# Kernel optimization log

Measured on AMD Instinct MI355X. Metric: run time of the kernel, lower is better.

## Reference

```python
import jax, jax.numpy as jnp
import numpy as np

N, E, C, H, L = 20000, 200000, 64, 4, 2
L0_IN, E_IN, L0_OUT = 65, 15, 64
HC = H * C
EPS = 1e-5  # InstanceNorm1d default eps
NEG_SLOPE = 0.01  # F.leaky_relu default used by DGL EGATConv


def setup_inputs() -> dict:
    key = jax.random.key(0)
    ks = jax.random.split(key, 16)
    def s(k, shape, fan):
        return (jax.random.normal(k, shape, jnp.float32) / np.float32(np.sqrt(fan)))
    return {
        "x": jax.random.normal(ks[0], (N, L0_IN), jnp.float32),
        "efeat": jax.random.normal(ks[1], (E, E_IN), jnp.float32),
        "src": jax.random.randint(ks[2], (E,), 0, N, dtype=jnp.int32),
        "dst": jax.random.randint(ks[3], (E,), 0, N, dtype=jnp.int32),
        "Wn0": s(ks[4], (L0_IN, C), L0_IN),
        "bn0": jnp.zeros((C,), jnp.float32),
        "We0": s(ks[5], (E_IN, C), E_IN),
        "be0": jnp.zeros((C,), jnp.float32),
        "Wnode": s(ks[6], (L, C, HC), C),
        "bnode": jnp.zeros((L, HC), jnp.float32),
        "Wni": s(ks[7], (L, C, HC), C),
        "Wnj": s(ks[8], (L, C, HC), C),
        "Wfij": s(ks[9], (L, C, HC), C),
        "attn": s(ks[10], (L, H, C), C),
        "bias_e": jnp.zeros((L, HC), jnp.float32),
        "Wf": s(ks[11], (C, L0_OUT), C),
        "bf": jnp.zeros((L0_OUT,), jnp.float32),
    }


def _inorm(x):
    # InstanceNorm1d on a 2D [rows, channels] tensor == per-row normalization
    m = jnp.mean(x, axis=-1, keepdims=True)
    v = jnp.var(x, axis=-1, keepdims=True)
    return (x - m) * jax.lax.rsqrt(v + EPS)


def reference(x, efeat, src, dst, Wn0, bn0, We0, be0, Wnode, bnode,
              Wni, Wnj, Wfij, attn, bias_e, Wf, bf):
    h = x @ Wn0 + bn0        # [N, C]
    f = efeat @ We0 + be0    # [E, C]
    for l in range(L):
        # edge feature update: f_out = fc_ni(h)[src] + fc_nj(h)[dst] + fc_fij(f) + bias
        f_out = (h @ Wni[l])[src] + (h @ Wnj[l])[dst] + f @ Wfij[l] + bias_e[l]  # [E, HC]
        e = jax.nn.leaky_relu(f_out, NEG_SLOPE).reshape(E, H, C)
        score = jnp.einsum('ehc,hc->eh', e, attn[l])  # [E, H]
        # edge softmax over incoming edges of each destination node
        smax = jax.ops.segment_max(score, dst, num_segments=N)
        w = jnp.exp(score - smax[dst])
        denom = jax.ops.segment_sum(w, dst, num_segments=N)
        a = w / denom[dst]                                # [E, H]
        hproj = (h @ Wnode[l] + bnode[l]).reshape(N, H, C)
        msg = hproj[src] * a[:, :, None]                  # [E, H, C]
        h_new = jax.ops.segment_sum(msg, dst, num_segments=N)  # [N, H, C]
        # mean over heads -> InstanceNorm -> ELU
        h = jax.nn.elu(_inorm(jnp.mean(h_new, axis=1)))
        f = jax.nn.elu(_inorm(jnp.mean(f_out.reshape(E, H, C), axis=1)))
    return h @ Wf + bf
```

## Files before the change

### kernel.cpp

```cpp
#include <hip/hip_runtime.h>
#include <cmath>

#define NN 20000
#define NE 200000
#define SCAN_BLOCKS 79
#define EBLK 3125
#define EBLK_P 391

typedef __attribute__((ext_vector_type(8))) short bf16x8;
typedef __attribute__((ext_vector_type(4))) float f32x4;
typedef unsigned int uint;

__device__ __forceinline__ float4 ld4(const float* p){ return *(const float4*)p; }

__device__ __forceinline__ uint packbf(float a, float b) {
  uint ua = __float_as_uint(a);
  uint ub = __float_as_uint(b);
  ua = (ua + 0x7fffu + ((ua >> 16) & 1u)) >> 16;
  ub = (ub + 0x7fffu + ((ub >> 16) & 1u)) >> 16;
  return ua | (ub << 16);
}
__device__ __forceinline__ float4 up4(uint2 u) {
  return make_float4(__uint_as_float(u.x << 16), __uint_as_float(u.x & 0xffff0000u),
                     __uint_as_float(u.y << 16), __uint_as_float(u.y & 0xffff0000u));
}

__global__ void gemm16_bf16(const float* __restrict__ A, const float* __restrict__ B,
                            const float* __restrict__ bias, uint2* __restrict__ O,
                            int M, int K, const int* __restrict__ map) {
  int idx = blockIdx.x * 256 + threadIdx.x;
  if (idx >= M * 4) return;
  int m = idx >> 2, jq = idx & 3;
  const float* a = A + (long)m * K;
  const float* b = B + jq * 16;
  float c00=0,c01=0,c02=0,c03=0,c04=0,c05=0,c06=0,c07=0;
  float c08=0,c09=0,c10=0,c11=0,c12=0,c13=0,c14=0,c15=0;
  for (int k = 0; k < K; k++) {
    float av = a[k];
    const float* br = b + (long)k * 64;
    float4 b0 = ld4(br), b1 = ld4(br + 4), b2 = ld4(br + 8), b3 = ld4(br + 12);
    c00 = fmaf(av, b0.x, c00); c01 = fmaf(av, b0.y, c01); c02 = fmaf(av, b0.z, c02); c03 = fmaf(av, b0.w, c03);
    c04 = fmaf(av, b1.x, c04); c05 = fmaf(av, b1.y, c05); c06 = fmaf(av, b1.z, c06); c07 = fmaf(av, b1.w, c07);
    c08 = fmaf(av, b2.x, c08); c09 = fmaf(av, b2.y, c09); c10 = fmaf(av, b2.z, c10); c11 = fmaf(av, b2.w, c11);
    c12 = fmaf(av, b3.x, c12); c13 = fmaf(av, b3.y, c13); c14 = fmaf(av, b3.z, c14); c15 = fmaf(av, b3.w, c15);
  }
  const float* bb = bias + jq * 16;
  float4 v0 = ld4(bb), v1 = ld4(bb + 4), v2 = ld4(bb + 8), v3 = ld4(bb + 12);
  int mo = map ? map[m] : m;
  uint2* op = O + (long)mo * 16 + jq * 4;
  op[0] = make_uint2(packbf(c00 + v0.x, c01 + v0.y), packbf(c02 + v0.z, c03 + v0.w));
  op[1] = make_uint2(packbf(c04 + v1.x, c05 + v1.y), packbf(c06 + v1.z, c07 + v1.w));
  op[2] = make_uint2(packbf(c08 + v2.x, c09 + v2.y), packbf(c10 + v2.z, c11 + v2.w));
  op[3] = make_uint2(packbf(c12 + v3.x, c13 + v3.y), packbf(c14 + v3.z, c15 + v3.w));
}

__global__ void zero_i32(int* __restrict__ p, int n) {
  int i = blockIdx.x * 256 + threadIdx.x;
  if (i < n) p[i] = 0;
}

__global__ void count_deg(const int* __restrict__ dst, int* __restrict__ deg) {
  int e = blockIdx.x * 256 + threadIdx.x;
  if (e < NE) atomicAdd(&deg[dst[e]], 1);
}

__global__ void scan1(const int* __restrict__ deg, int* __restrict__ off, int* __restrict__ bsum) {
  __shared__ int buf[256];
  int t = threadIdx.x;
  int g = blockIdx.x * 256 + t;
  int v = (g < NN) ? deg[g] : 0;
  buf[t] = v;
  __syncthreads();
  for (int s = 1; s < 256; s <<= 1) {
    int x = (t >= s) ? buf[t - s] : 0;
    __syncthreads();
    buf[t] += x;
    __syncthreads();
  }
  if (g < NN) off[g] = buf[t] - v;
  if (t == 255) bsum[blockIdx.x] = buf[255];
}

__global__ void scan2(int* __restrict__ bsum, int* __restrict__ off) {
  __shared__ int buf[128];
  int t = threadIdx.x;
  int v = (t < SCAN_BLOCKS) ? bsum[t] : 0;
  buf[t] = v;
  __syncthreads();
  for (int s = 1; s < 128; s <<= 1) {
    int x = (t >= s) ? buf[t - s] : 0;
    __syncthreads();
    buf[t] += x;
    __syncthreads();
  }
  if (t < SCAN_BLOCKS) bsum[t] = buf[t] - v;
  if (t == 127) off[NN] = buf[127];
}

__global__ void scan3(int* __restrict__ off, const int* __restrict__ bsum) {
  int g = blockIdx.x * 256 + threadIdx.x;
  if (g < NN) off[g] += bsum[blockIdx.x];
}

__global__ void fill_csr(const int* __restrict__ dst, const int* __restrict__ src,
                         const int* __restrict__ off, int* __restrict__ cursor,
                         int* __restrict__ esrc, int* __restrict__ edst,
                         int* __restrict__ csr_pos) {
  int e = blockIdx.x * 256 + threadIdx.x;
  if (e >= NE) return;
  int d = dst[e];
  int p = atomicAdd(&cursor[d], 1);
  int pos = off[d] + p;
  esrc[pos] = src[e];
  edst[pos] = d;
  csr_pos[e] = pos;
}

__global__ void prep_w(const float* __restrict__ Wni, const float* __restrict__ Wnj,
                       const float* __restrict__ Wfij, const float* __restrict__ Wnode,
                       const float* __restrict__ bnode,
                       uint* __restrict__ Wcat, uint* __restrict__ WcT,
                       float* __restrict__ bmean) {
  int rid = blockIdx.x * 256 + threadIdx.x;
  if (rid < 512) {
    int l = rid >> 8, c = rid & 255;
    uint* D = Wcat + (size_t)l * 24576 + c * 96;
    for (int k8 = 0; k8 < 24; k8++) {
      int ss = k8 >> 3;
      const float* S = (ss == 0 ? Wni : ss == 1 ? Wnj : Wfij) + l * 16384;
      int kl = (k8 & 7) * 8;
      uint u0 = packbf(S[(kl+0)*256 + c], S[(kl+1)*256 + c]);
      uint u1 = packbf(S[(kl+2)*256 + c], S[(kl+3)*256 + c]);
      uint u2 = packbf(S[(kl+4)*256 + c], S[(kl+5)*256 + c]);
      uint u3 = packbf(S[(kl+6)*256 + c], S[(kl+7)*256 + c]);
      *((uint4*)(D + k8 * 4)) = make_uint4(u0, u1, u2, u3);
    }
  } else if (rid < 640) {
    int idx = rid - 512;
    int l = idx >> 6, c = idx & 63;
    const float* S = Wnode + l * 16384;
    uint* D = WcT + (size_t)l * 8192 + c * 128;
    for (int kp = 0; kp < 128; kp++) {
      int k0 = kp * 2, k1 = kp * 2 + 1;
      float v0 = S[(k0 & 63) * 256 + (k0 >> 6) * 64 + c] * 0.25f;
      float v1 = S[(k1 & 63) * 256 + (k1 >> 6) * 64 + c] * 0.25f;
      D[kp] = packbf(v0, v1);
    }
  } else if (rid < 768) {
    int idx = rid - 640;
    int l = idx >> 6, c = idx & 63;
    const float* S = bnode + l * 256;
    bmean[l * 64 + c] = 0.25f * (S[c] + S[64 + c] + S[128 + c] + S[192 + c]);
  }
}

__global__ __launch_bounds__(256) void edge_mfma(
    const uint4* __restrict__ f_bf, const uint4* __restrict__ h_bf,
    const uint* __restrict__ Wcat_l, const float* __restrict__ be_l,
    const float* __restrict__ attn_l, const int* __restrict__ esrc,
    const int* __restrict__ edst, float* __restrict__ scc,
    uint2* __restrict__ f_next)
{
  int nb = (blockIdx.x & 7) * EBLK_P + (blockIdx.x >> 3);
  if (nb >= EBLK) return;
  int base = nb * 64;
  __shared__ float red[4][2][33][6];
  int t = threadIdx.x, lane = t & 63, w = t >> 6;
  int col = lane & 15, quad = lane >> 4;
  float4 be4[4], at4[4];
  #pragma unroll
  for (int hg = 0; hg < 4; hg++) {
    int ce = (4 * hg + w) * 16 + quad * 4;
    be4[hg] = ld4(be_l + ce);
    at4[hg] = ld4(attn_l + ce);
  }
  float ma[2][2][4];
  #pragma unroll 1
  for (int ch = 0; ch < 2; ch++) {
    int ea = base + ch * 32 + col;
    int eb = ea + 16;
    int sa = esrc[ea], da = edst[ea];
    int sb = esrc[eb], db = edst[eb];
    bf16x8 Ba[6], Bb[6];
    Ba[0] = *(const bf16x8*)&h_bf[(long)sa * 8 + quad];
    Ba[1] = *(const bf16x8*)&h_bf[(long)sa * 8 + 4 + quad];
    Ba[2] = *(const bf16x8*)&h_bf[(long)da * 8 + quad];
    Ba[3] = *(const bf16x8*)&h_bf[(long)da * 8 + 4 + quad];
    Ba[4] = *(const bf16x8*)&f_bf[(long)ea * 8 + quad];
    Ba[5] = *(const bf16x8*)&f_bf[(long)ea * 8 + 4 + quad];
    Bb[0] = *(const bf16x8*)&h_bf[(long)sb * 8 + quad];
    Bb[1] = *(const bf16x8*)&h_bf[(long)sb * 8 + 4 + quad];
    Bb[2] = *(const bf16x8*)&h_bf[(long)db * 8 + quad];
    Bb[3] = *(const bf16x8*)&h_bf[(long)db * 8 + 4 + quad];
    Bb[4] = *(const bf16x8*)&f_bf[(long)eb * 8 + quad];
    Bb[5] = *(const bf16x8*)&f_bf[(long)eb * 8 + 4 + quad];
    float ma0 = 0.f, ma1 = 0.f, ma2 = 0.f, ma3 = 0.f;
    float mb0 = 0.f, mb1 = 0.f, mb2 = 0.f, mb3 = 0.f;
    float sa0 = 0.f, sa1 = 0.f, sa2 = 0.f, sa3 = 0.f;
    float sb0 = 0.f, sb1 = 0.f, sb2 = 0.f, sb3 = 0.f;
    #pragma unroll
    for (int hg = 0; hg < 4; hg++) {
      f32x4 aa = (f32x4){0.f, 0.f, 0.f, 0.f};
      f32x4 ab = (f32x4){0.f, 0.f, 0.f, 0.f};
      const uint* Ab = &Wcat_l[((4 * hg + w) * 16 + col) * 96 + quad * 4];
      #pragma unroll
      for (int kt = 0; kt < 6; kt++) {
        bf16x8 Af = *(const bf16x8*)(Ab + kt * 16);
        aa = __builtin_amdgcn_mfma_f32_16x16x32_bf16(Af, Ba[kt], aa, 0, 0, 0);
        ab = __builtin_amdgcn_mfma_f32_16x16x32_bf16(Af, Bb[kt], ab, 0, 0, 0);
      }
      float xa0 = aa[0] + be4[hg].x, xa1 = aa[1] + be4[hg].y;
      float xa2 = aa[2] + be4[hg].z, xa3 = aa[3] + be4[hg].w;
      float xb0 = ab[0] + be4[hg].x, xb1 = ab[1] + be4[hg].y;
      float xb2 = ab[2] + be4[hg].z, xb3 = ab[3] + be4[hg].w;
      float la0 = xa0 > 0.f ? xa0 : 0.01f * xa0;
      float la1 = xa1 > 0.f ? xa1 : 0.01f * xa1;
      float la2 = xa2 > 0.f ? xa2 : 0.01f * xa2;
      float la3 = xa3 > 0.f ? xa3 : 0.01f * xa3;
      float lb0 = xb0 > 0.f ? xb0 : 0.01f * xb0;
      float lb1 = xb1 > 0.f ? xb1 : 0.01f * xb1;
      float lb2 = xb2 > 0.f ? xb2 : 0.01f * xb2;
      float lb3 = xb3 > 0.f ? xb3 : 0.01f * xb3;
      float dpa = la0 * at4[hg].x + la1 * at4[hg].y + la2 * at4[hg].z + la3 * at4[hg].w;
      float dpb = lb0 * at4[hg].x + lb1 * at4[hg].y + lb2 * at4[hg].z + lb3 * at4[hg].w;
      if (hg == 0) { sa0 = dpa; sb0 = dpb; }
      else if (hg == 1) { sa1 = dpa; sb1 = dpb; }
      else if (hg == 2) { sa2 = dpa; sb2 = dpb; }
      else { sa3 = dpa; sb3 = dpb; }
      ma0 += xa0; ma1 += xa1; ma2 += xa2; ma3 += xa3;
      mb0 += xb0; mb1 += xb1; mb2 += xb2; mb3 += xb3;
    }
    ma0 *= 0.25f; ma1 *= 0.25f; ma2 *= 0.25f; ma3 *= 0.25f;
    mb0 *= 0.25f; mb1 *= 0.25f; mb2 *= 0.25f; mb3 *= 0.25f;
    ma[ch][0][0] = ma0; ma[ch][0][1] = ma1; ma[ch][0][2] = ma2; ma[ch][0][3] = ma3;
    ma[ch][1][0] = mb0; ma[ch][1][1] = mb1; ma[ch][1][2] = mb2; ma[ch][1][3] = mb3;
    float s1a = ma0 + ma1 + ma2 + ma3;
    float s2a = ma0*ma0 + ma1*ma1 + ma2*ma2 + ma3*ma3;
    float s1b = mb0 + mb1 + mb2 + mb3;
    float s2b = mb0*mb0 + mb1*mb1 + mb2*mb2 + mb3*mb3;
    sa0 += __shfl_xor(sa0, 16); sa0 += __shfl_xor(sa0, 32);
    sa1 += __shfl_xor(sa1, 16); sa1 += __shfl_xor(sa1, 32);
    sa2 += __shfl_xor(sa2, 16); sa2 += __shfl_xor(sa2, 32);
    sa3 += __shfl_xor(sa3, 16); sa3 += __shfl_xor(sa3, 32);
    sb0 += __shfl_xor(sb0, 16); sb0 += __shfl_xor(sb0, 32);
    sb1 += __shfl_xor(sb1, 16); sb1 += __shfl_xor(sb1, 32);
    sb2 += __shfl_xor(sb2, 16); sb2 += __shfl_xor(sb2, 32);
    sb3 += __shfl_xor(sb3, 16); sb3 += __shfl_xor(sb3, 32);
    s1a += __shfl_xor(s1a, 16); s1a += __shfl_xor(s1a, 32);
    s2a += __shfl_xor(s2a, 16); s2a += __shfl_xor(s2a, 32);
    s1b += __shfl_xor(s1b, 16); s1b += __shfl_xor(s1b, 32);
    s2b += __shfl_xor(s2b, 16); s2b += __shfl_xor(s2b, 32);
    if (quad == 0) {
      float* ra = &red[w][ch][col][0];
      ra[0] = sa0; ra[1] = sa1; ra[2] = sa2; ra[3] = sa3; ra[4] = s1a; ra[5] = s2a;
      float* rb = &red[w][ch][16 + col][0];
      rb[0] = sb0; rb[1] = sb1; rb[2] = sb2; rb[3] = sb3; rb[4] = s1b; rb[5] = s2b;
    }
  }
  __syncthreads();
  {
    int eL = t >> 2, hh = t & 3;
    int chx = eL >> 5, c32 = eL & 31;
    float sv = red[0][chx][c32][hh] + red[1][chx][c32][hh]
             + red[2][chx][c32][hh] + red[3][chx][c32][hh];
    scc[(long)(base + eL) * 4 + hh] = sv;
  }
  #pragma unroll
  for (int ch = 0; ch < 2; ch++) {
    #pragma unroll
    for (int sub = 0; sub < 2; sub++) {
      int c32 = sub * 16 + col;
      int e = base + ch * 32 + c32;
      float s1T = red[0][ch][c32][4] + red[1][ch][c32][4]
                + red[2][ch][c32][4] + red[3][ch][c32][4];
      float s2T = red[0][ch][c32][5] + red[1][ch][c32][5]
                + red[2][ch][c32][5] + red[3][ch][c32][5];
      float mean = s1T * 0.015625f;
      float var  = s2T * 0.015625f - mean * mean;
      float rs = rsqrtf(var + 1e-5f);
      float o0 = (ma[ch][sub][0] - mean) * rs; o0 = o0 > 0.f ? o0 : expm1f(o0);
      float o1 = (ma[ch][sub][1] - mean) * rs; o1 = o1 > 0.f ? o1 : expm1f(o1);
      float o2 = (ma[ch][sub][2] - mean) * rs; o2 = o2 > 0.f ? o2 : expm1f(o2);
      float o3 = (ma[ch][sub][3] - mean) * rs; o3 = o3 > 0.f ? o3 : expm1f(o3);
      f_next[(long)e * 16 + w * 4 + quad] = make_uint2(packbf(o0, o1), packbf(o2, o3));
    }
  }
}

__global__ __launch_bounds__(256) void agg_combine(
    const uint* __restrict__ h_u, const float4* __restrict__ sc_csr4,
    const int* __restrict__ esrc, const int* __restrict__ off,
    const uint4* __restrict__ WcT4, const float* __restrict__ bmean_l,
    uint2* __restrict__ h_next)
{
  __shared__ uint gsh[16][132];
  __shared__ float red2[4][17][2];
  int t = threadIdx.x, lane = t & 63, w = t >> 6;
  int col = lane & 15, quad = lane >> 4;
  int half = lane >> 5, seg = lane & 31;
  int n0 = blockIdx.x * 16;
  bf16x8 A2[8];
  #pragma unroll
  for (int kt = 0; kt < 8; kt++)
    A2[kt] = *(const bf16x8*)&WcT4[(w * 16 + col) * 32 + kt * 4 + quad];
  #pragma unroll 1
  for (int nl = 0; nl < 4; nl++) {
    int n = n0 + w * 4 + nl;
    int o0 = off[n], o1 = off[n + 1];
    uint u0 = 0u, u1 = 0u, u2 = 0u, u3 = 0u;
    if (o0 < o1) {
      float mx0 = -3.0e38f, mx1 = -3.0e38f, mx2 = -3.0e38f, mx3 = -3.0e38f;
      for (int i = o0 + half; i < o1; i += 2) {
        float4 s = sc_csr4[i];
        mx0 = fmaxf(mx0, s.x); mx1 = fmaxf(mx1, s.y);
        mx2 = fmaxf(mx2, s.z); mx3 = fmaxf(mx3, s.w);
      }
      mx0 = fmaxf(mx0, __shfl_xor(mx0, 32)); mx1 = fmaxf(mx1, __shfl_xor(mx1, 32));
      mx2 = fmaxf(mx2, __shfl_xor(mx2, 32)); mx3 = fmaxf(mx3, __shfl_xor(mx3, 32));
      float d0 = 0.f, d1 = 0.f, d2 = 0.f, d3 = 0.f;
      float a00=0.f,a01=0.f,a10=0.f,a11=0.f,a20=0.f,a21=0.f,a30=0.f,a31=0.f;
      for (int i = o0 + half; i < o1; i += 2) {
        float4 s = sc_csr4[i];
        float w0 = __expf(s.x - mx0), w1 = __expf(s.y - mx1);
        float w2 = __expf(s.z - mx2), w3 = __expf(s.w - mx3);
        d0 += w0; d1 += w1; d2 += w2; d3 += w3;
        int sr = esrc[i];
        uint hv = h_u[(long)sr * 32 + seg];
        float hlo = __uint_as_float(hv << 16);
        float hhi = __uint_as_float(hv & 0xffff0000u);
        a00 = fmaf(w0, hlo, a00); a01 = fmaf(w0, hhi, a01);
        a10 = fmaf(w1, hlo, a10); a11 = fmaf(w1, hhi, a11);
        a20 = fmaf(w2, hlo, a20); a21 = fmaf(w2, hhi, a21);
        a30 = fmaf(w3, hlo, a30); a31 = fmaf(w3, hhi, a31);
      }
      d0 += __shfl_xor(d0, 32); d1 += __shfl_xor(d1, 32);
      d2 += __shfl_xor(d2, 32); d3 += __shfl_xor(d3, 32);
      a00 += __shfl_xor(a00, 32); a01 += __shfl_xor(a01, 32);
      a10 += __shfl_xor(a10, 32); a11 += __shfl_xor(a11, 32);
      a20 += __shfl_xor(a20, 32); a21 += __shfl_xor(a21, 32);
      a30 += __shfl_xor(a30, 32); a31 += __shfl_xor(a31, 32);
      float i0 = 1.f / d0, i1 = 1.f / d1, i2 = 1.f / d2, i3 = 1.f / d3;
      u0 = packbf(a00 * i0, a01 * i0);
      u1 = packbf(a10 * i1, a11 * i1);
      u2 = packbf(a20 * i2, a21 * i2);
      u3 = packbf(a30 * i3, a31 * i3);
    }
    int nloc = w * 4 + nl;
    if (half == 0) { gsh[nloc][seg] = u0; gsh[nloc][32 + seg] = u1; }
    else           { gsh[nloc][64 + seg] = u2; gsh[nloc][96 + seg] = u3; }
  }
  __syncthreads();
  f32x4 acc = (f32x4){0.f, 0.f, 0.f, 0.f};
  #pragma unroll
  for (int kt = 0; kt < 8; kt++) {
    bf16x8 Bg = *(const bf16x8*)&gsh[col][kt * 16 + quad * 4];
    acc = __builtin_amdgcn_mfma_f32_16x16x32_bf16(A2[kt], Bg, acc, 0, 0, 0);
  }
  int n2 = n0 + col;
  int dg = off[n2 + 1] - off[n2];
  float4 bm = ld4(bmean_l + w * 16 + quad * 4);
  float x0, x1, x2, x3;
  if (dg > 0) { x0 = acc[0] + bm.x; x1 = acc[1] + bm.y; x2 = acc[2] + bm.z; x3 = acc[3] + bm.w; }
  else { x0 = x1 = x2 = x3 = 0.f; }
  float s1 = x0 + x1 + x2 + x3;
  float s2 = x0*x0 + x1*x1 + x2*x2 + x3*x3;
  s1 += __shfl_xor(s1, 16); s2 += __shfl_xor(s2, 16);
  s1 += __shfl_xor(s1, 32); s2 += __shfl_xor(s2, 32);
  if (quad == 0) { red2[w][col][0] = s1; red2[w][col][1] = s2; }
  __syncthreads();
  float s1T = red2[0][col][0] + red2[1][col][0] + red2[2][col][0] + red2[3][col][0];
  float s2T = red2[0][col][1] + red2[1][col][1] + red2[2][col][1] + red2[3][col][1];
  float mean = s1T * 0.015625f;
  float var  = s2T * 0.015625f - mean * mean;
  float rs = rsqrtf(var + 1e-5f);
  float o0 = (x0 - mean) * rs; o0 = o0 > 0.f ? o0 : expm1f(o0);
  float o1 = (x1 - mean) * rs; o1 = o1 > 0.f ? o1 : expm1f(o1);
  float o2 = (x2 - mean) * rs; o2 = o2 > 0.f ? o2 : expm1f(o2);
  float o3 = (x3 - mean) * rs; o3 = o3 > 0.f ? o3 : expm1f(o3);
  h_next[(long)n2 * 16 + w * 4 + quad] = make_uint2(packbf(o0, o1), packbf(o2, o3));
}

__global__ void final_gemm(const uint2* __restrict__ h, const float* __restrict__ Wf,
                           const float* __restrict__ bf_, float* __restrict__ out) {
  int idx = blockIdx.x * 256 + threadIdx.x;
  if (idx >= NN * 16) return;
  int m = idx >> 4, j4 = (idx & 15) << 2;
  const uint2* row = h + (long)m * 16;
  float ax = 0.f, ay = 0.f, az = 0.f, aw = 0.f;
  for (int kk = 0; kk < 16; kk++) {
    float4 a = up4(row[kk]);
    float4 b0 = ld4(Wf + (kk * 4 + 0) * 64 + j4);
    float4 b1 = ld4(Wf + (kk * 4 + 1) * 64 + j4);
    float4 b2 = ld4(Wf + (kk * 4 + 2) * 64 + j4);
    float4 b3 = ld4(Wf + (kk * 4 + 3) * 64 + j4);
    ax = fmaf(a.x, b0.x, ax); ay = fmaf(a.x, b0.y, ay); az = fmaf(a.x, b0.z, az); aw = fmaf(a.x, b0.w, aw);
    ax = fmaf(a.y, b1.x, ax); ay = fmaf(a.y, b1.y, ay); az = fmaf(a.y, b1.z, az); aw = fmaf(a.y, b1.w, aw);
    ax = fmaf(a.z, b2.x, ax); ay = fmaf(a.z, b2.y, ay); az = fmaf(a.z, b2.z, az); aw = fmaf(a.z, b2.w, aw);
    ax = fmaf(a.w, b3.x, ax); ay = fmaf(a.w, b3.y, ay); az = fmaf(a.w, b3.z, az); aw = fmaf(a.w, b3.w, aw);
  }
  float4 bb = ld4(bf_ + j4);
  *(float4*)(out + (long)m * 64 + j4) = make_float4(ax + bb.x, ay + bb.y, az + bb.z, aw + bb.w);
}

extern "C" void kernel_launch(void* const* d_in, const int* in_sizes, int n_in,
                              void* d_out, int out_size, void* d_ws, size_t ws_size,
                              hipStream_t stream) {
  const float* x      = (const float*)d_in[0];
  const float* efeat  = (const float*)d_in[1];
  const int*   src    = (const int*)d_in[2];
  const int*   dst    = (const int*)d_in[3];
  const float* Wn0    = (const float*)d_in[4];
  const float* bn0    = (const float*)d_in[5];
  const float* We0    = (const float*)d_in[6];
  const float* be0    = (const float*)d_in[7];
  const float* Wnode  = (const float*)d_in[8];
  const float* bnode  = (const float*)d_in[9];
  const float* Wni    = (const float*)d_in[10];
  const float* Wnj    = (const float*)d_in[11];
  const float* Wfij   = (const float*)d_in[12];
  const float* attn   = (const float*)d_in[13];
  const float* bias_e = (const float*)d_in[14];
  const float* Wf     = (const float*)d_in[15];
  const float* bf     = (const float*)d_in[16];
  float* out = (float*)d_out;

  char* w = (char*)d_ws;
  auto alloc = [&](size_t nbytes) { char* p = w; w += (nbytes + 255) & ~(size_t)255; return p; };
  uint2* h_a   = (uint2*)alloc((size_t)NN * 128);
  uint2* h_b   = (uint2*)alloc((size_t)NN * 128);
  uint2* f_a   = (uint2*)alloc((size_t)NE * 128);
  uint2* f_b   = (uint2*)alloc((size_t)NE * 128);
  float* scc   = (float*)alloc((size_t)NE * 16);
  uint*  Wcat  = (uint*)alloc((size_t)2 * 24576 * 4);
  uint*  WcT   = (uint*)alloc((size_t)2 * 8192 * 4);
  float* bmean = (float*)alloc((size_t)2 * 64 * 4);
  int* deg     = (int*)alloc((size_t)NN * 2 * 4);
  int* cursor  = deg + NN;
  int* off     = (int*)alloc((size_t)(NN + 1) * 4);
  int* esrc    = (int*)alloc((size_t)NE * 4);
  int* edst    = (int*)alloc((size_t)NE * 4);
  int* csr_pos = (int*)alloc((size_t)NE * 4);
  int* bsum    = (int*)alloc((size_t)128 * 4);

  zero_i32<<<(2 * NN + 255) / 256, 256, 0, stream>>>(deg, 2 * NN);
  count_deg<<<(NE + 255) / 256, 256, 0, stream>>>(dst, deg);
  scan1<<<SCAN_BLOCKS, 256, 0, stream>>>(deg, off, bsum);
  scan2<<<1, 128, 0, stream>>>(bsum, off);
  scan3<<<SCAN_BLOCKS, 256, 0, stream>>>(off, bsum);
  fill_csr<<<(NE + 255) / 256, 256, 0, stream>>>(dst, src, off, cursor, esrc, edst, csr_pos);

  gemm16_bf16<<<(NN * 4 + 255) / 256, 256, 0, stream>>>(x, Wn0, bn0, h_a, NN, 65, nullptr);
  gemm16_bf16<<<(NE * 4 + 255) / 256, 256, 0, stream>>>(efeat, We0, be0, f_a, NE, 15, csr_pos);
  prep_w<<<4, 256, 0, stream>>>(Wni, Wnj, Wfij, Wnode, bnode, Wcat, WcT, bmean);

  uint2* hc = h_a; uint2* hn = h_b;
  uint2* fc = f_a; uint2* fn = f_b;
  for (int l = 0; l < 2; l++) {
    const uint* Wcat_l = Wcat + (size_t)l * 24576;
    const uint4* WcT_l = (const uint4*)(WcT + (size_t)l * 8192);
    const float* bm_l  = bmean + (size_t)l * 64;
    const float* be_l  = bias_e + (size_t)l * 256;
    const float* at_l  = attn + (size_t)l * 256;
    edge_mfma<<<8 * EBLK_P, 256, 0, stream>>>((const uint4*)fc, (const uint4*)hc,
                                              Wcat_l, be_l, at_l, esrc, edst, scc, fn);
    agg_combine<<<NN / 16, 256, 0, stream>>>((const uint*)hc, (const float4*)scc,
                                             esrc, off, WcT_l, bm_l, hn);
    uint2* tmp = hc; hc = hn; hn = tmp;
    tmp = fc; fc = fn; fn = tmp;
  }
  final_gemm<<<(NN * 16 + 255) / 256, 256, 0, stream>>>(hc, Wf, bf, out);
}
```

Baseline: 521.9 us.

## Stage edge gathers through LDS, coalesce feature stores, widen aggregation gathers

The edge kernel now gathers source, destination and edge feature rows cooperatively with full 16-byte loads into a shared staging buffer. The second chunk's gather is issued early so it overlaps the first chunk's MFMA work. Edge and node outputs are written to shared memory first and then stored to global memory as coalesced 16-byte vectors. The aggregation kernel splits each node's edges across four quads that each read 8-byte node slices, then reduces with shuffles. This adds shared memory, extra barriers and more shuffle work in exchange for fewer, wider memory transactions.

```diff
diff --git a/kernel.cpp b/kernel.cpp
--- a/kernel.cpp
+++ b/kernel.cpp
@@ -159,41 +159,47 @@
     const uint* __restrict__ Wcat_l, const float* __restrict__ be_l,
     const float* __restrict__ attn_l, const int* __restrict__ esrc,
     const int* __restrict__ edst, float* __restrict__ scc,
-    uint2* __restrict__ f_next)
+    uint4* __restrict__ f_next4)
 {
   int nb = (blockIdx.x & 7) * EBLK_P + (blockIdx.x >> 3);
   if (nb >= EBLK) return;
   int base = nb * 64;
+  __shared__ uint bstage[2][96 * 36];
   __shared__ float red[4][2][33][6];
   int t = threadIdx.x, lane = t & 63, w = t >> 6;
   int col = lane & 15, quad = lane >> 4;
-  float4 be4[4], at4[4];
+  int sr = t >> 3, sc = t & 7;
+  {
+    int e0 = base + sr;
+    uint4 vs = h_bf[(long)esrc[e0] * 8 + sc];
+    uint4 vd = h_bf[(long)edst[e0] * 8 + sc];
+    uint4 vf = f_bf[(long)e0 * 8 + sc];
+    *(uint4*)&bstage[0][sr * 36 + sc * 4] = vs;
+    *(uint4*)&bstage[0][(32 + sr) * 36 + sc * 4] = vd;
+    *(uint4*)&bstage[0][(64 + sr) * 36 + sc * 4] = vf;
+  }
+  int e1 = base + 32 + sr;
+  uint4 v1s = h_bf[(long)esrc[e1] * 8 + sc];
+  uint4 v1d = h_bf[(long)edst[e1] * 8 + sc];
+  uint4 v1f = f_bf[(long)e1 * 8 + sc];
+  __syncthreads();
+  float ma[2][2][4];
   #pragma unroll
-  for (int hg = 0; hg < 4; hg++) {
-    int ce = (4 * hg + w) * 16 + quad * 4;
-    be4[hg] = ld4(be_l + ce);
-    at4[hg] = ld4(attn_l + ce);
-  }
-  float ma[2][2][4];
-  #pragma unroll 1
   for (int ch = 0; ch < 2; ch++) {
-    int ea = base + ch * 32 + col;
-    int eb = ea + 16;
-    int sa = esrc[ea], da = edst[ea];
-    int sb = esrc[eb], db = edst[eb];
+    const uint* bp = &bstage[ch][0];
     bf16x8 Ba[6], Bb[6];
-    Ba[0] = *(const bf16x8*)&h_bf[(long)sa * 8 + quad];
-    Ba[1] = *(const bf16x8*)&h_bf[(long)sa * 8 + 4 + quad];
-    Ba[2] = *(const bf16x8*)&h_bf[(long)da * 8 + quad];
-    Ba[3] = *(const bf16x8*)&h_bf[(long)da * 8 + 4 + quad];
-    Ba[4] = *(const bf16x8*)&f_bf[(long)ea * 8 + quad];
-    Ba[5] = *(const bf16x8*)&f_bf[(long)ea * 8 + 4 + quad];
-    Bb[0] = *(const bf16x8*)&h_bf[(long)sb * 8 + quad];
-    Bb[1] = *(const bf16x8*)&h_bf[(long)sb * 8 + 4 + quad];
-    Bb[2] = *(const bf16x8*)&h_bf[(long)db * 8 + quad];
-    Bb[3] = *(const bf16x8*)&h_bf[(long)db * 8 + 4 + quad];
-    Bb[4] = *(const bf16x8*)&f_bf[(long)eb * 8 + quad];
-    Bb[5] = *(const bf16x8*)&f_bf[(long)eb * 8 + 4 + quad];
+    Ba[0] = *(const bf16x8*)&bp[col * 36 + quad * 4];
+    Ba[1] = *(const bf16x8*)&bp[col * 36 + 16 + quad * 4];
+    Ba[2] = *(const bf16x8*)&bp[(32 + col) * 36 + quad * 4];
+    Ba[3] = *(const bf16x8*)&bp[(32 + col) * 36 + 16 + quad * 4];
+    Ba[4] = *(const bf16x8*)&bp[(64 + col) * 36 + quad * 4];
+    Ba[5] = *(const bf16x8*)&bp[(64 + col) * 36 + 16 + quad * 4];
+    Bb[0] = *(const bf16x8*)&bp[(16 + col) * 36 + quad * 4];
+    Bb[1] = *(const bf16x8*)&bp[(16 + col) * 36 + 16 + quad * 4];
+    Bb[2] = *(const bf16x8*)&bp[(48 + col) * 36 + quad * 4];
+    Bb[3] = *(const bf16x8*)&bp[(48 + col) * 36 + 16 + quad * 4];
+    Bb[4] = *(const bf16x8*)&bp[(80 + col) * 36 + quad * 4];
+    Bb[5] = *(const bf16x8*)&bp[(80 + col) * 36 + 16 + quad * 4];
     float ma0 = 0.f, ma1 = 0.f, ma2 = 0.f, ma3 = 0.f;
     float mb0 = 0.f, mb1 = 0.f, mb2 = 0.f, mb3 = 0.f;
     float sa0 = 0.f, sa1 = 0.f, sa2 = 0.f, sa3 = 0.f;
@@ -209,10 +215,13 @@
         aa = __builtin_amdgcn_mfma_f32_16x16x32_bf16(Af, Ba[kt], aa, 0, 0, 0);
         ab = __builtin_amdgcn_mfma_f32_16x16x32_bf16(Af, Bb[kt], ab, 0, 0, 0);
       }
-      float xa0 = aa[0] + be4[hg].x, xa1 = aa[1] + be4[hg].y;
-      float xa2 = aa[2] + be4[hg].z, xa3 = aa[3] + be4[hg].w;
-      float xb0 = ab[0] + be4[hg].x, xb1 = ab[1] + be4[hg].y;
-      float xb2 = ab[2] + be4[hg].z, xb3 = ab[3] + be4[hg].w;
+      int ce = (4 * hg + w) * 16 + quad * 4;
+      float4 be4 = ld4(be_l + ce);
+      float4 at4 = ld4(attn_l + ce);
+      float xa0 = aa[0] + be4.x, xa1 = aa[1] + be4.y;
+      float xa2 = aa[2] + be4.z, xa3 = aa[3] + be4.w;
+      float xb0 = ab[0] + be4.x, xb1 = ab[1] + be4.y;
+      float xb2 = ab[2] + be4.z, xb3 = ab[3] + be4.w;
       float la0 = xa0 > 0.f ? xa0 : 0.01f * xa0;
       float la1 = xa1 > 0.f ? xa1 : 0.01f * xa1;
       float la2 = xa2 > 0.f ? xa2 : 0.01f * xa2;
@@ -221,8 +230,8 @@
       float lb1 = xb1 > 0.f ? xb1 : 0.01f * xb1;
       float lb2 = xb2 > 0.f ? xb2 : 0.01f * xb2;
       float lb3 = xb3 > 0.f ? xb3 : 0.01f * xb3;
-      float dpa = la0 * at4[hg].x + la1 * at4[hg].y + la2 * at4[hg].z + la3 * at4[hg].w;
-      float dpb = lb0 * at4[hg].x + lb1 * at4[hg].y + lb2 * at4[hg].z + lb3 * at4[hg].w;
+      float dpa = la0 * at4.x + la1 * at4.y + la2 * at4.z + la3 * at4.w;
+      float dpb = lb0 * at4.x + lb1 * at4.y + lb2 * at4.z + lb3 * at4.w;
       if (hg == 0) { sa0 = dpa; sb0 = dpb; }
       else if (hg == 1) { sa1 = dpa; sb1 = dpb; }
       else if (hg == 2) { sa2 = dpa; sb2 = dpb; }
@@ -256,6 +265,12 @@
       float* rb = &red[w][ch][16 + col][0];
       rb[0] = sb0; rb[1] = sb1; rb[2] = sb2; rb[3] = sb3; rb[4] = s1b; rb[5] = s2b;
     }
+    if (ch == 0) {
+      *(uint4*)&bstage[1][sr * 36 + sc * 4] = v1s;
+      *(uint4*)&bstage[1][(32 + sr) * 36 + sc * 4] = v1d;
+      *(uint4*)&bstage[1][(64 + sr) * 36 + sc * 4] = v1f;
+      __syncthreads();
+    }
   }
   __syncthreads();
   {
@@ -265,12 +280,12 @@
              + red[2][chx][c32][hh] + red[3][chx][c32][hh];
     scc[(long)(base + eL) * 4 + hh] = sv;
   }
+  uint* fout = &bstage[0][0];
   #pragma unroll
   for (int ch = 0; ch < 2; ch++) {
     #pragma unroll
     for (int sub = 0; sub < 2; sub++) {
       int c32 = sub * 16 + col;
-      int e = base + ch * 32 + c32;
       float s1T = red[0][ch][c32][4] + red[1][ch][c32][4]
                 + red[2][ch][c32][4] + red[3][ch][c32][4];
       float s2T = red[0][ch][c32][5] + red[1][ch][c32][5]
@@ -282,22 +297,33 @@
       float o1 = (ma[ch][sub][1] - mean) * rs; o1 = o1 > 0.f ? o1 : expm1f(o1);
       float o2 = (ma[ch][sub][2] - mean) * rs; o2 = o2 > 0.f ? o2 : expm1f(o2);
       float o3 = (ma[ch][sub][3] - mean) * rs; o3 = o3 > 0.f ? o3 : expm1f(o3);
-      f_next[(long)e * 16 + w * 4 + quad] = make_uint2(packbf(o0, o1), packbf(o2, o3));
-    }
+      int eL = ch * 32 + c32;
+      fout[eL * 36 + w * 8 + quad * 2]     = packbf(o0, o1);
+      fout[eL * 36 + w * 8 + quad * 2 + 1] = packbf(o2, o3);
+    }
+  }
+  __syncthreads();
+  {
+    int row = t >> 2, part = t & 3;
+    uint4 x0 = *(uint4*)&fout[row * 36 + part * 8];
+    uint4 x1 = *(uint4*)&fout[row * 36 + part * 8 + 4];
+    long gp = ((long)(base + row)) * 8 + part * 2;
+    f_next4[gp] = x0;
+    f_next4[gp + 1] = x1;
   }
 }
 
 __global__ __launch_bounds__(256) void agg_combine(
-    const uint* __restrict__ h_u, const float4* __restrict__ sc_csr4,
+    const uint2* __restrict__ h2, const float4* __restrict__ sc_csr4,
     const int* __restrict__ esrc, const int* __restrict__ off,
     const uint4* __restrict__ WcT4, const float* __restrict__ bmean_l,
-    uint2* __restrict__ h_next)
+    uint4* __restrict__ h_next4)
 {
   __shared__ uint gsh[16][132];
   __shared__ float red2[4][17][2];
+  __shared__ uint fout2[16 * 36];
   int t = threadIdx.x, lane = t & 63, w = t >> 6;
   int col = lane & 15, quad = lane >> 4;
-  int half = lane >> 5, seg = lane & 31;
   int n0 = blockIdx.x * 16;
   bf16x8 A2[8];
   #pragma unroll
@@ -307,47 +333,66 @@
   for (int nl = 0; nl < 4; nl++) {
     int n = n0 + w * 4 + nl;
     int o0 = off[n], o1 = off[n + 1];
-    uint u0 = 0u, u1 = 0u, u2 = 0u, u3 = 0u;
+    float mx0 = -3.0e38f, mx1 = -3.0e38f, mx2 = -3.0e38f, mx3 = -3.0e38f;
+    for (int i = o0 + quad; i < o1; i += 4) {
+      float4 s = sc_csr4[i];
+      mx0 = fmaxf(mx0, s.x); mx1 = fmaxf(mx1, s.y);
+      mx2 = fmaxf(mx2, s.z); mx3 = fmaxf(mx3, s.w);
+    }
+    mx0 = fmaxf(mx0, __shfl_xor(mx0, 16)); mx0 = fmaxf(mx0, __shfl_xor(mx0, 32));
+    mx1 = fmaxf(mx1, __shfl_xor(mx1, 16)); mx1 = fmaxf(mx1, __shfl_xor(mx1, 32));
+    mx2 = fmaxf(mx2, __shfl_xor(mx2, 16)); mx2 = fmaxf(mx2, __shfl_xor(mx2, 32));
+    mx3 = fmaxf(mx3, __shfl_xor(mx3, 16)); mx3 = fmaxf(mx3, __shfl_xor(mx3, 32));
+    float d0 = 0.f, d1 = 0.f, d2 = 0.f, d3 = 0.f;
+    float a00=0.f,a01=0.f,a02=0.f,a03=0.f, a10=0.f,a11=0.f,a12=0.f,a13=0.f;
+    float a20=0.f,a21=0.f,a22=0.f,a23=0.f, a30=0.f,a31=0.f,a32=0.f,a33=0.f;
+    for (int i = o0 + quad; i < o1; i += 4) {
+      float4 s = sc_csr4[i];
+      float w0 = __expf(s.x - mx0), w1 = __expf(s.y - mx1);
+      float w2 = __expf(s.z - mx2), w3 = __expf(s.w - mx3);
+      d0 += w0; d1 += w1; d2 += w2; d3 += w3;
+      uint2 hv = h2[(long)esrc[i] * 16 + col];
+      float4 p = up4(hv);
+      a00 = fmaf(w0,p.x,a00); a01 = fmaf(w0,p.y,a01); a02 = fmaf(w0,p.z,a02); a03 = fmaf(w0,p.w,a03);
+      a10 = fmaf(w1,p.x,a10); a11 = fmaf(w1,p.y,a11); a12 = fmaf(w1,p.z,a12); a13 = fmaf(w1,p.w,a13);
+      a20 = fmaf(w2,p.x,a20); a21 = fmaf(w2,p.y,a21); a22 = fmaf(w2,p.z,a22); a23 = fmaf(w2,p.w,a23);
+      a30 = fmaf(w3,p.x,a30); a31 = fmaf(w3,p.y,a31); a32 = fmaf(w3,p.z,a32); a33 = fmaf(w3,p.w,a33);
+    }
+    d0 += __shfl_xor(d0,16); d0 += __shfl_xor(d0,32);
+    d1 += __shfl_xor(d1,16); d1 += __shfl_xor(d1,32);
+    d2 += __shfl_xor(d2,16); d2 += __shfl_xor(d2,32);
+    d3 += __shfl_xor(d3,16); d3 += __shfl_xor(d3,32);
+    a00 += __shfl_xor(a00,16); a00 += __shfl_xor(a00,32);
+    a01 += __shfl_xor(a01,16); a01 += __shfl_xor(a01,32);
+    a02 += __shfl_xor(a02,16); a02 += __shfl_xor(a02,32);
+    a03 += __shfl_xor(a03,16); a03 += __shfl_xor(a03,32);
+    a10 += __shfl_xor(a10,16); a10 += __shfl_xor(a10,32);
+    a11 += __shfl_xor(a11,16); a11 += __shfl_xor(a11,32);
+    a12 += __shfl_xor(a12,16); a12 += __shfl_xor(a12,32);
+    a13 += __shfl_xor(a13,16); a13 += __shfl_xor(a13,32);
+    a20 += __shfl_xor(a20,16); a20 += __shfl_xor(a20,32);
+    a21 += __shfl_xor(a21,16); a21 += __shfl_xor(a21,32);
+    a22 += __shfl_xor(a22,16); a22 += __shfl_xor(a22,32);
+    a23 += __shfl_xor(a23,16); a23 += __shfl_xor(a23,32);
+    a30 += __shfl_xor(a30,16); a30 += __shfl_xor(a30,32);
+    a31 += __shfl_xor(a31,16); a31 += __shfl_xor(a31,32);
+    a32 += __shfl_xor(a32,16); a32 += __shfl_xor(a32,32);
+    a33 += __shfl_xor(a33,16); a33 += __shfl_xor(a33,32);
+    uint u0 = 0u, u1 = 0u, u2 = 0u, u3 = 0u, u4 = 0u, u5 = 0u, u6 = 0u, u7 = 0u;
     if (o0 < o1) {
-      float mx0 = -3.0e38f, mx1 = -3.0e38f, mx2 = -3.0e38f, mx3 = -3.0e38f;
-      for (int i = o0 + half; i < o1; i += 2) {
-        float4 s = sc_csr4[i];
-        mx0 = fmaxf(mx0, s.x); mx1 = fmaxf(mx1, s.y);
-        mx2 = fmaxf(mx2, s.z); mx3 = fmaxf(mx3, s.w);
-      }
-      mx0 = fmaxf(mx0, __shfl_xor(mx0, 32)); mx1 = fmaxf(mx1, __shfl_xor(mx1, 32));
-      mx2 = fmaxf(mx2, __shfl_xor(mx2, 32)); mx3 = fmaxf(mx3, __shfl_xor(mx3, 32));
-      float d0 = 0.f, d1 = 0.f, d2 = 0.f, d3 = 0.f;
-      float a00=0.f,a01=0.f,a10=0.f,a11=0.f,a20=0.f,a21=0.f,a30=0.f,a31=0.f;
-      for (int i = o0 + half; i < o1; i += 2) {
-        float4 s = sc_csr4[i];
-        float w0 = __expf(s.x - mx0), w1 = __expf(s.y - mx1);
-        float w2 = __expf(s.z - mx2), w3 = __expf(s.w - mx3);
-        d0 += w0; d1 += w1; d2 += w2; d3 += w3;
-        int sr = esrc[i];
-        uint hv = h_u[(long)sr * 32 + seg];
-        float hlo = __uint_as_float(hv << 16);
-        float hhi = __uint_as_float(hv & 0xffff0000u);
-        a00 = fmaf(w0, hlo, a00); a01 = fmaf(w0, hhi, a01);
-        a10 = fmaf(w1, hlo, a10); a11 = fmaf(w1, hhi, a11);
-        a20 = fmaf(w2, hlo, a20); a21 = fmaf(w2, hhi, a21);
-        a30 = fmaf(w3, hlo, a30); a31 = fmaf(w3, hhi, a31);
-      }
-      d0 += __shfl_xor(d0, 32); d1 += __shfl_xor(d1, 32);
-      d2 += __shfl_xor(d2, 32); d3 += __shfl_xor(d3, 32);
-      a00 += __shfl_xor(a00, 32); a01 += __shfl_xor(a01, 32);
-      a10 += __shfl_xor(a10, 32); a11 += __shfl_xor(a11, 32);
-      a20 += __shfl_xor(a20, 32); a21 += __shfl_xor(a21, 32);
-      a30 += __shfl_xor(a30, 32); a31 += __shfl_xor(a31, 32);
       float i0 = 1.f / d0, i1 = 1.f / d1, i2 = 1.f / d2, i3 = 1.f / d3;
-      u0 = packbf(a00 * i0, a01 * i0);
-      u1 = packbf(a10 * i1, a11 * i1);
-      u2 = packbf(a20 * i2, a21 * i2);
-      u3 = packbf(a30 * i3, a31 * i3);
-    }
-    int nloc = w * 4 + nl;
-    if (half == 0) { gsh[nloc][seg] = u0; gsh[nloc][32 + seg] = u1; }
-    else           { gsh[nloc][64 + seg] = u2; gsh[nloc][96 + seg] = u3; }
+      u0 = packbf(a00*i0, a01*i0); u1 = packbf(a02*i0, a03*i0);
+      u2 = packbf(a10*i1, a11*i1); u3 = packbf(a12*i1, a13*i1);
+      u4 = packbf(a20*i2, a21*i2); u5 = packbf(a22*i2, a23*i2);
+      u6 = packbf(a30*i3, a31*i3); u7 = packbf(a32*i3, a33*i3);
+    }
+    if (quad == 0) {
+      int nloc = w * 4 + nl;
+      gsh[nloc][col*2]      = u0; gsh[nloc][col*2 + 1]      = u1;
+      gsh[nloc][32 + col*2] = u2; gsh[nloc][32 + col*2 + 1] = u3;
+      gsh[nloc][64 + col*2] = u4; gsh[nloc][64 + col*2 + 1] = u5;
+      gsh[nloc][96 + col*2] = u6; gsh[nloc][96 + col*2 + 1] = u7;
+    }
   }
   __syncthreads();
   f32x4 acc = (f32x4){0.f, 0.f, 0.f, 0.f};
@@ -377,7 +422,14 @@
   float o1 = (x1 - mean) * rs; o1 = o1 > 0.f ? o1 : expm1f(o1);
   float o2 = (x2 - mean) * rs; o2 = o2 > 0.f ? o2 : expm1f(o2);
   float o3 = (x3 - mean) * rs; o3 = o3 > 0.f ? o3 : expm1f(o3);
-  h_next[(long)n2 * 16 + w * 4 + quad] = make_uint2(packbf(o0, o1), packbf(o2, o3));
+  fout2[col * 36 + w * 8 + quad * 2]     = packbf(o0, o1);
+  fout2[col * 36 + w * 8 + quad * 2 + 1] = packbf(o2, o3);
+  __syncthreads();
+  if (t < 128) {
+    int row = t >> 3, part = t & 7;
+    uint4 x = *(uint4*)&fout2[row * 36 + part * 4];
+    h_next4[((long)(n0 + row)) * 8 + part] = x;
+  }
 }
 
 __global__ void final_gemm(const uint2* __restrict__ h, const float* __restrict__ Wf,
@@ -462,9 +514,10 @@
     const float* be_l  = bias_e + (size_t)l * 256;
     const float* at_l  = attn + (size_t)l * 256;
     edge_mfma<<<8 * EBLK_P, 256, 0, stream>>>((const uint4*)fc, (const uint4*)hc,
-                                              Wcat_l, be_l, at_l, esrc, edst, scc, fn);
-    agg_combine<<<NN / 16, 256, 0, stream>>>((const uint*)hc, (const float4*)scc,
-                                             esrc, off, WcT_l, bm_l, hn);
+                                              Wcat_l, be_l, at_l, esrc, edst, scc,
+                                              (uint4*)fn);
+    agg_combine<<<NN / 16, 256, 0, stream>>>((const uint2*)hc, (const float4*)scc,
+                                             esrc, off, WcT_l, bm_l, (uint4*)hn);
     uint2* tmp = hc; hc = hn; hn = tmp;
     tmp = fc; fc = fn; fn = tmp;
   }
```

Result: faster. 499.5 us (-4.3%).
